# Performance work log

Hardware: AMD Instinct MI355X
Metric: run time of the kernel (lower is better)

Reference implementation:

```python
import jax, jax.numpy as jnp
import numpy as np

B, IN, H, OUT = 4096, 1024, 1024, 1024


def setup_inputs() -> dict:
    key = jax.random.key(0)
    ks = jax.random.split(key, 16)
    s_in = 1.0 / np.sqrt(IN)
    s_h = 1.0 / np.sqrt(H)
    d = {}
    d['input_vec'] = jax.random.normal(ks[0], (B, IN), jnp.float32)
    d['hidden_vec'] = jax.random.normal(ks[1], (B, H), jnp.float32)
    d['cell_vec'] = jax.random.normal(ks[2], (B, H), jnp.float32)
    names = ['f', 'i', 'o', 'g']
    for j, n in enumerate(names):
        d['Wx_' + n] = jax.random.uniform(ks[3 + 3 * j], (H, IN), jnp.float32, -s_in, s_in)
        d['bx_' + n] = jax.random.uniform(ks[4 + 3 * j], (H,), jnp.float32, -s_in, s_in)
        d['Wh_' + n] = jax.random.uniform(ks[5 + 3 * j], (H, H), jnp.float32, -s_h, s_h)
    d['W_out'] = jax.random.uniform(ks[15], (OUT, H), jnp.float32, -s_h, s_h)
    d['b_out'] = jax.random.uniform(jax.random.fold_in(key, 99), (OUT,), jnp.float32, -s_h, s_h)
    return d


def reference(input_vec, hidden_vec, cell_vec,
              Wx_f, bx_f, Wh_f,
              Wx_i, bx_i, Wh_i,
              Wx_o, bx_o, Wh_o,
              Wx_g, bx_g, Wh_g,
              W_out, b_out):
    # Fuse the 8 small linears into two GEMMs: [B,IN]x[IN,4H] and [B,H]x[H,4H].
    Wx = jnp.concatenate([Wx_f, Wx_i, Wx_o, Wx_g], axis=0)   # [4H, IN]
    Wh = jnp.concatenate([Wh_f, Wh_i, Wh_o, Wh_g], axis=0)   # [4H, H]
    b = jnp.concatenate([bx_f, bx_i, bx_o, bx_g], axis=0)    # [4H]
    gates = input_vec @ Wx.T + hidden_vec @ Wh.T + b          # [B, 4H]
    f, i, o, g = jnp.split(gates, 4, axis=1)
    f = jax.nn.sigmoid(f)
    i = jax.nn.sigmoid(i)
    o = jax.nn.sigmoid(o)
    g = jnp.tanh(g)
    new_cell = f * cell_vec + i * g
    new_hidden = o * jnp.tanh(new_cell)
    output_vec = new_hidden @ W_out.T + b_out
    return (new_hidden, new_cell, output_vec)
```

## Files before the change

### kernel.cpp

```cpp
#include <hip/hip_runtime.h>
#include <hip/hip_bf16.h>
#include <stdint.h>

#define B_   4096
#define IN_  1024
#define H_   1024
#define OUT_ 1024

typedef __attribute__((ext_vector_type(8)))  short short8;
typedef __attribute__((ext_vector_type(16))) float floatx16;

__device__ static inline void gload_lds16(const void* g, void* l) {
    __builtin_amdgcn_global_load_lds(
        (const __attribute__((address_space(1))) unsigned int*)g,
        (__attribute__((address_space(3))) unsigned int*)l,
        16, 0, 0);
}

__device__ static inline float sigmoidf_(float x) { return 1.0f / (1.0f + __expf(-x)); }
__device__ static inline float tanhf_(float x)    { return 1.0f - 2.0f / (1.0f + __expf(2.0f * x)); }

struct Ptrs8 { const float* p[8]; };

__global__ void cvt_all_kernel(const float* __restrict__ x, const float* __restrict__ h,
                               Ptrs8 ptrs, const float* __restrict__ wout,
                               __hip_bfloat16* __restrict__ xh,
                               __hip_bfloat16* __restrict__ Wc,
                               __hip_bfloat16* __restrict__ Wob) {
    int blk = blockIdx.x;
    const float* src;
    __hip_bfloat16* dst;
    if (blk < 8192) {
        int idx = blk * 256 + threadIdx.x;
        int b  = idx >> 9;
        int c4 = (idx & 511) * 4;
        src = (c4 < IN_) ? (x + (size_t)b * IN_ + c4)
                         : (h + (size_t)b * H_ + (c4 - IN_));
        dst = xh + (size_t)b * 2048 + c4;
    } else if (blk < 16384) {
        int idx = (blk - 8192) * 256 + threadIdx.x;
        int n  = idx >> 9;
        int c4 = (idx & 511) * 4;
        int gate = (n >> 5) & 3;
        int hh   = ((n >> 7) << 5) + (n & 31);
        src = (c4 < 1024) ? (ptrs.p[2 * gate]     + (size_t)hh * 1024 + c4)
                          : (ptrs.p[2 * gate + 1] + (size_t)hh * 1024 + (c4 - 1024));
        dst = Wc + (size_t)n * 2048 + c4;
    } else {
        int idx = (blk - 16384) * 256 + threadIdx.x;
        src = wout + (size_t)idx * 4;
        dst = Wob + (size_t)idx * 4;
    }
    float4 v = *(const float4*)src;
    dst[0] = __float2bfloat16(v.x);
    dst[1] = __float2bfloat16(v.y);
    dst[2] = __float2bfloat16(v.z);
    dst[3] = __float2bfloat16(v.w);
}

__global__ __launch_bounds__(512, 2) void gemm_gate_fused(
    const __hip_bfloat16* __restrict__ A,
    const __hip_bfloat16* __restrict__ Bm,
    const float* __restrict__ cell,
    const float* __restrict__ bxf, const float* __restrict__ bxi,
    const float* __restrict__ bxo, const float* __restrict__ bxg,
    float* __restrict__ new_hidden, float* __restrict__ new_cell,
    __hip_bfloat16* __restrict__ hb)
{
    constexpr int K = 2048;

    __shared__ short sA0[16384];
    __shared__ short sB0[16384];
    __shared__ short sA1[16384];
    __shared__ short sB1[16384];

    const int tid  = threadIdx.x;
    const int lane = tid & 63;
    const int wv   = tid >> 6;
    const int wr   = wv >> 1;
    const int wc   = wv & 1;

    const int bid    = blockIdx.x;
    const int xcd    = bid & 7;
    const int loc    = bid >> 3;
    const int n_tile = xcd * 2 + (loc & 1);
    const int m_tile = loc >> 1;
    const int m0 = m_tile * 256;
    const int n0 = n_tile * 256;

    const int srow   = tid >> 3;
    const int schunk = tid & 7;
    const int scg    = schunk ^ (srow & 7);
    const __hip_bfloat16* Ag = A  + (size_t)(m0 + srow) * K + scg * 8;
    const __hip_bfloat16* Bg = Bm + (size_t)(n0 + srow) * K + scg * 8;
    const int wvoff = wv * 1024;

    const int fr    = lane & 31;
    const int khalf = lane >> 5;
    const int sw    = fr & 7;

    int offA[2], offB[4];
    #pragma unroll
    for (int i = 0; i < 2; ++i) offA[i] = (wr * 64 + i * 32 + fr) * 128;
    #pragma unroll
    for (int j = 0; j < 4; ++j) offB[j] = (wc * 128 + j * 32 + fr) * 128;

    floatx16 acc[2][4] = {};

    #pragma unroll
    for (int s = 0; s < 4; ++s)
        gload_lds16(Ag + (size_t)(s * 64) * K, (char*)sA0 + s * 8192 + wvoff);
    #pragma unroll
    for (int s = 0; s < 4; ++s)
        gload_lds16(Bg + (size_t)(s * 64) * K, (char*)sB0 + s * 8192 + wvoff);
    asm volatile("s_waitcnt vmcnt(0)" ::: "memory");
    __builtin_amdgcn_s_barrier();
    __builtin_amdgcn_sched_barrier(0);

    auto tile_body = [&](const short* RA, const short* RB, short* WA, short* WB,
                         const __hip_bfloat16* Agt, const __hip_bfloat16* Bgt,
                         bool do_stage) {
        #pragma unroll
        for (int kk = 0; kk < 4; ++kk) {
            if (do_stage) {
                if (kk == 0) {
                    gload_lds16(Agt,                    (char*)WA + 0 * 8192 + wvoff);
                    gload_lds16(Agt + (size_t)64 * K,   (char*)WA + 1 * 8192 + wvoff);
                    gload_lds16(Bgt,                    (char*)WB + 0 * 8192 + wvoff);
                    gload_lds16(Bgt + (size_t)64 * K,   (char*)WB + 1 * 8192 + wvoff);
                } else if (kk == 1) {
                    gload_lds16(Agt + (size_t)128 * K,  (char*)WA + 2 * 8192 + wvoff);
                    gload_lds16(Agt + (size_t)192 * K,  (char*)WA + 3 * 8192 + wvoff);
                    gload_lds16(Bgt + (size_t)128 * K,  (char*)WB + 2 * 8192 + wvoff);
                    gload_lds16(Bgt + (size_t)192 * K,  (char*)WB + 3 * 8192 + wvoff);
                }
            }

            const int co = ((kk * 2 + khalf) ^ sw) * 16;
            short8 af[2], bfr[4];
            #pragma unroll
            for (int i = 0; i < 2; ++i)
                af[i] = *(const short8*)((const char*)RA + offA[i] + co);
            #pragma unroll
            for (int j = 0; j < 4; ++j)
                bfr[j] = *(const short8*)((const char*)RB + offB[j] + co);

            __builtin_amdgcn_s_barrier();
            __builtin_amdgcn_s_setprio(1);
            #pragma unroll
            for (int i = 0; i < 2; ++i)
                #pragma unroll
                for (int j = 0; j < 4; ++j)
                    acc[i][j] = __builtin_amdgcn_mfma_f32_32x32x16_bf16(af[i], bfr[j], acc[i][j], 0, 0, 0);
            __builtin_amdgcn_s_setprio(0);
            if (kk == 3)
                asm volatile("s_waitcnt vmcnt(0)" ::: "memory");
            __builtin_amdgcn_s_barrier();
            if (kk == 3)
                __builtin_amdgcn_sched_barrier(0);
        }
    };

    #pragma unroll 1
    for (int t2 = 0; t2 < 16; ++t2) {
        const int te = 2 * t2;
        tile_body(sA0, sB0, sA1, sB1,
                  Ag + (size_t)(te + 1) * 64, Bg + (size_t)(te + 1) * 64, true);
        tile_body(sA1, sB1, sA0, sB0,
                  Ag + (size_t)(te + 2) * 64, Bg + (size_t)(te + 2) * 64, t2 < 15);
    }

    const int h  = ((n0 + wc * 128) >> 2) + fr;
    const float bfb = bxf[h];
    const float bib = bxi[h];
    const float bob = bxo[h];
    const float bgb = bxg[h];

    #pragma unroll
    for (int i = 0; i < 2; ++i) {
        const int row_base = m0 + wr * 64 + i * 32 + 4 * khalf;
        #pragma unroll
        for (int reg = 0; reg < 16; ++reg) {
            const int row = row_base + (reg & 3) + 8 * (reg >> 2);
            const size_t off = (size_t)row * H_ + h;
            const float f  = sigmoidf_(acc[i][0][reg] + bfb);
            const float ii = sigmoidf_(acc[i][1][reg] + bib);
            const float o  = sigmoidf_(acc[i][2][reg] + bob);
            const float g  = tanhf_(acc[i][3][reg] + bgb);
            const float c  = f * cell[off] + ii * g;
            const float nh = o * tanhf_(c);
            new_cell[off]   = c;
            new_hidden[off] = nh;
            hb[off] = __float2bfloat16(nh);
        }
    }
}

__global__ __launch_bounds__(256, 2) void gemm_out(
    const __hip_bfloat16* __restrict__ A,
    const __hip_bfloat16* __restrict__ Bm,
    float* __restrict__ C,
    const float* __restrict__ bias)
{
    constexpr int BK = 64;
    constexpr int K  = 1024;
    constexpr int N  = 1024;

    __shared__ __hip_bfloat16 ldsA[128 * BK];
    __shared__ __hip_bfloat16 ldsB[64 * BK];

    const int tid  = threadIdx.x;
    const int lane = tid & 63;
    const int wv   = tid >> 6;

    const int bid    = blockIdx.x;
    const int xcd    = bid & 7;
    const int loc    = bid >> 3;
    const int n_tile = xcd * 2 + (loc & 1);
    const int m_tile = loc >> 1;
    const int m0 = m_tile * 128;
    const int n0 = n_tile * 64;

    const int srow   = tid >> 3;
    const int schunk = tid & 7;
    const int scg    = schunk ^ (srow & 7);
    const __hip_bfloat16* Ag = A  + (size_t)(m0 + srow) * K + scg * 8;
    const __hip_bfloat16* Bg = Bm + (size_t)(n0 + srow) * K + scg * 8;
    char* lA = (char*)ldsA + wv * 1024;
    char* lB = (char*)ldsB + wv * 1024;

    const int wrow  = wv * 32;
    const int fr    = lane & 31;
    const int khalf = lane >> 5;

    floatx16 acc[2] = {};

    for (int k0 = 0; k0 < K; k0 += BK) {
        #pragma unroll
        for (int s = 0; s < 4; ++s)
            gload_lds16(Ag + (size_t)(s * 32) * K + k0, lA + s * 4096);
        #pragma unroll
        for (int s = 0; s < 2; ++s)
            gload_lds16(Bg + (size_t)(s * 32) * K + k0, lB + s * 4096);
        __syncthreads();

        #pragma unroll
        for (int kk = 0; kk < 4; ++kk) {
            const int cg = kk * 2 + khalf;
            const int ra = wrow + fr;
            short8 af = *(const short8*)((const char*)ldsA + ra * 128 + ((cg ^ (ra & 7)) * 16));
            short8 bf[2];
            #pragma unroll
            for (int j = 0; j < 2; ++j) {
                const int r = j * 32 + fr;
                bf[j] = *(const short8*)((const char*)ldsB + r * 128 + ((cg ^ (r & 7)) * 16));
            }
            #pragma unroll
            for (int j = 0; j < 2; ++j)
                acc[j] = __builtin_amdgcn_mfma_f32_32x32x16_bf16(af, bf[j], acc[j], 0, 0, 0);
        }
        __syncthreads();
    }

    #pragma unroll
    for (int j = 0; j < 2; ++j) {
        const int col = n0 + j * 32 + fr;
        const float bb = bias[col];
        #pragma unroll
        for (int reg = 0; reg < 16; ++reg) {
            const int row = m0 + wrow + 4 * khalf + (reg & 3) + 8 * (reg >> 2);
            C[(size_t)row * N + col] = acc[j][reg] + bb;
        }
    }
}

extern "C" void kernel_launch(void* const* d_in, const int* in_sizes, int n_in,
                              void* d_out, int out_size, void* d_ws, size_t ws_size,
                              hipStream_t stream) {
    const float* input_vec  = (const float*)d_in[0];
    const float* hidden_vec = (const float*)d_in[1];
    const float* cell_vec   = (const float*)d_in[2];
    const float* Wx_f = (const float*)d_in[3];
    const float* bx_f = (const float*)d_in[4];
    const float* Wh_f = (const float*)d_in[5];
    const float* Wx_i = (const float*)d_in[6];
    const float* bx_i = (const float*)d_in[7];
    const float* Wh_i = (const float*)d_in[8];
    const float* Wx_o = (const float*)d_in[9];
    const float* bx_o = (const float*)d_in[10];
    const float* Wh_o = (const float*)d_in[11];
    const float* Wx_g = (const float*)d_in[12];
    const float* bx_g = (const float*)d_in[13];
    const float* Wh_g = (const float*)d_in[14];
    const float* W_out = (const float*)d_in[15];
    const float* b_out = (const float*)d_in[16];

    char* ws = (char*)d_ws;
    __hip_bfloat16* xh  = (__hip_bfloat16*)(ws);
    __hip_bfloat16* Wc  = (__hip_bfloat16*)(ws + (16ull << 20));
    __hip_bfloat16* Wob = (__hip_bfloat16*)(ws + (32ull << 20));
    __hip_bfloat16* hb  = (__hip_bfloat16*)(ws + (34ull << 20));

    float* new_hidden = (float*)d_out;
    float* new_cell   = new_hidden + (size_t)B_ * H_;
    float* out_vec    = new_cell + (size_t)B_ * H_;

    Ptrs8 p;
    p.p[0] = Wx_f; p.p[1] = Wh_f; p.p[2] = Wx_i; p.p[3] = Wh_i;
    p.p[4] = Wx_o; p.p[5] = Wh_o; p.p[6] = Wx_g; p.p[7] = Wh_g;
    cvt_all_kernel<<<17408, 256, 0, stream>>>(input_vec, hidden_vec, p, W_out, xh, Wc, Wob);

    gemm_gate_fused<<<256, 512, 0, stream>>>(
        xh, Wc, cell_vec, bx_f, bx_i, bx_o, bx_g, new_hidden, new_cell, hb);

    gemm_out<<<512, 256, 0, stream>>>(hb, Wob, out_vec, b_out);
}
```

Measured before the change: 249.8 us.

## Use 4 waves with 128x128 per-wave tiles and one barrier per K-tile

The gate GEMM now launches 256 threads instead of 512, and each wave accumulates a 128x128 output block with a 4x4 grid of MFMA accumulators instead of 2x4. All global-to-LDS staging for the next K-tile is issued at the start of each tile body, and the per-kk barriers and priority switches are replaced by a single wait-and-barrier at the end of each tile. The aim is more register-level reuse of LDS fragments and less synchronisation overhead. The cost is much higher register pressure, fewer waves available to hide latency, and the launch bounds drop to one block per CU.

```diff
diff --git a/kernel.cpp b/kernel.cpp
--- a/kernel.cpp
+++ b/kernel.cpp
@@ -58,7 +58,7 @@
     dst[3] = __float2bfloat16(v.w);
 }
 
-__global__ __launch_bounds__(512, 2) void gemm_gate_fused(
+__global__ __launch_bounds__(256, 1) void gemm_gate_fused(
     const __hip_bfloat16* __restrict__ A,
     const __hip_bfloat16* __restrict__ Bm,
     const float* __restrict__ cell,
@@ -99,76 +99,63 @@
     const int khalf = lane >> 5;
     const int sw    = fr & 7;
 
-    int offA[2], offB[4];
-    #pragma unroll
-    for (int i = 0; i < 2; ++i) offA[i] = (wr * 64 + i * 32 + fr) * 128;
+    int offA[4], offB[4];
+    #pragma unroll
+    for (int i = 0; i < 4; ++i) offA[i] = (wr * 128 + i * 32 + fr) * 128;
     #pragma unroll
     for (int j = 0; j < 4; ++j) offB[j] = (wc * 128 + j * 32 + fr) * 128;
 
-    floatx16 acc[2][4] = {};
-
-    #pragma unroll
-    for (int s = 0; s < 4; ++s)
-        gload_lds16(Ag + (size_t)(s * 64) * K, (char*)sA0 + s * 8192 + wvoff);
-    #pragma unroll
-    for (int s = 0; s < 4; ++s)
-        gload_lds16(Bg + (size_t)(s * 64) * K, (char*)sB0 + s * 8192 + wvoff);
+    floatx16 acc[4][4] = {};
+
+    #pragma unroll
+    for (int s = 0; s < 8; ++s) {
+        gload_lds16(Ag + (size_t)(s * 32) * K, (char*)sA0 + s * 4096 + wvoff);
+        gload_lds16(Bg + (size_t)(s * 32) * K, (char*)sB0 + s * 4096 + wvoff);
+    }
     asm volatile("s_waitcnt vmcnt(0)" ::: "memory");
     __builtin_amdgcn_s_barrier();
     __builtin_amdgcn_sched_barrier(0);
 
-    auto tile_body = [&](const short* RA, const short* RB, short* WA, short* WB,
-                         const __hip_bfloat16* Agt, const __hip_bfloat16* Bgt,
-                         bool do_stage) {
-        #pragma unroll
-        for (int kk = 0; kk < 4; ++kk) {
-            if (do_stage) {
-                if (kk == 0) {
-                    gload_lds16(Agt,                    (char*)WA + 0 * 8192 + wvoff);
-                    gload_lds16(Agt + (size_t)64 * K,   (char*)WA + 1 * 8192 + wvoff);
-                    gload_lds16(Bgt,                    (char*)WB + 0 * 8192 + wvoff);
-                    gload_lds16(Bgt + (size_t)64 * K,   (char*)WB + 1 * 8192 + wvoff);
-                } else if (kk == 1) {
-                    gload_lds16(Agt + (size_t)128 * K,  (char*)WA + 2 * 8192 + wvoff);
-                    gload_lds16(Agt + (size_t)192 * K,  (char*)WA + 3 * 8192 + wvoff);
-                    gload_lds16(Bgt + (size_t)128 * K,  (char*)WB + 2 * 8192 + wvoff);
-                    gload_lds16(Bgt + (size_t)192 * K,  (char*)WB + 3 * 8192 + wvoff);
-                }
-            }
-
-            const int co = ((kk * 2 + khalf) ^ sw) * 16;
-            short8 af[2], bfr[4];
-            #pragma unroll
-            for (int i = 0; i < 2; ++i)
-                af[i] = *(const short8*)((const char*)RA + offA[i] + co);
-            #pragma unroll
-            for (int j = 0; j < 4; ++j)
-                bfr[j] = *(const short8*)((const char*)RB + offB[j] + co);
-
-            __builtin_amdgcn_s_barrier();
-            __builtin_amdgcn_s_setprio(1);
-            #pragma unroll
-            for (int i = 0; i < 2; ++i)
-                #pragma unroll
-                for (int j = 0; j < 4; ++j)
-                    acc[i][j] = __builtin_amdgcn_mfma_f32_32x32x16_bf16(af[i], bfr[j], acc[i][j], 0, 0, 0);
-            __builtin_amdgcn_s_setprio(0);
-            if (kk == 3)
-                asm volatile("s_waitcnt vmcnt(0)" ::: "memory");
-            __builtin_amdgcn_s_barrier();
-            if (kk == 3)
-                __builtin_amdgcn_sched_barrier(0);
-        }
-    };
+#define TILE_BODY(RA, RB, WA, WB, tnext, DO_STAGE)                                        \
+    {                                                                                     \
+        if (DO_STAGE) {                                                                   \
+            const __hip_bfloat16* Agt = Ag + (size_t)(tnext) * 64;                        \
+            const __hip_bfloat16* Bgt = Bg + (size_t)(tnext) * 64;                        \
+            _Pragma("unroll")                                                             \
+            for (int s = 0; s < 8; ++s) {                                                 \
+                gload_lds16(Agt + (size_t)(s * 32) * K, (char*)(WA) + s * 4096 + wvoff);  \
+                gload_lds16(Bgt + (size_t)(s * 32) * K, (char*)(WB) + s * 4096 + wvoff);  \
+            }                                                                             \
+            __builtin_amdgcn_sched_barrier(0);                                            \
+        }                                                                                 \
+        _Pragma("unroll")                                                                 \
+        for (int kk = 0; kk < 4; ++kk) {                                                  \
+            const int co = ((kk * 2 + khalf) ^ sw) * 16;                                  \
+            short8 af[4], bfr[4];                                                         \
+            _Pragma("unroll")                                                             \
+            for (int i = 0; i < 4; ++i)                                                   \
+                af[i]  = *(const short8*)((const char*)(RA) + offA[i] + co);              \
+            _Pragma("unroll")                                                             \
+            for (int j = 0; j < 4; ++j)                                                   \
+                bfr[j] = *(const short8*)((const char*)(RB) + offB[j] + co);              \
+            _Pragma("unroll")                                                             \
+            for (int i = 0; i < 4; ++i)                                                   \
+                _Pragma("unroll")                                                         \
+                for (int j = 0; j < 4; ++j)                                               \
+                    acc[i][j] = __builtin_amdgcn_mfma_f32_32x32x16_bf16(                  \
+                        af[i], bfr[j], acc[i][j], 0, 0, 0);                               \
+        }                                                                                 \
+        asm volatile("s_waitcnt vmcnt(0)" ::: "memory");                                  \
+        __builtin_amdgcn_s_barrier();                                                     \
+        __builtin_amdgcn_sched_barrier(0);                                                \
+    }
 
     #pragma unroll 1
     for (int t2 = 0; t2 < 16; ++t2) {
-        const int te = 2 * t2;
-        tile_body(sA0, sB0, sA1, sB1,
-                  Ag + (size_t)(te + 1) * 64, Bg + (size_t)(te + 1) * 64, true);
-        tile_body(sA1, sB1, sA0, sB0,
-                  Ag + (size_t)(te + 2) * 64, Bg + (size_t)(te + 2) * 64, t2 < 15);
-    }
+        TILE_BODY(sA0, sB0, sA1, sB1, 2 * t2 + 1, true);
+        TILE_BODY(sA1, sB1, sA0, sB0, 2 * t2 + 2, (t2 < 15));
+    }
+#undef TILE_BODY
 
     const int h  = ((n0 + wc * 128) >> 2) + fr;
     const float bfb = bxf[h];
@@ -177,8 +164,8 @@
     const float bgb = bxg[h];
 
     #pragma unroll
-    for (int i = 0; i < 2; ++i) {
-        const int row_base = m0 + wr * 64 + i * 32 + 4 * khalf;
+    for (int i = 0; i < 4; ++i) {
+        const int row_base = m0 + wr * 128 + i * 32 + 4 * khalf;
         #pragma unroll
         for (int reg = 0; reg < 16; ++reg) {
             const int row = row_base + (reg & 3) + 8 * (reg >> 2);
@@ -310,7 +297,7 @@
     p.p[4] = Wx_o; p.p[5] = Wh_o; p.p[6] = Wx_g; p.p[7] = Wh_g;
     cvt_all_kernel<<<17408, 256, 0, stream>>>(input_vec, hidden_vec, p, W_out, xh, Wc, Wob);
 
-    gemm_gate_fused<<<256, 512, 0, stream>>>(
+    gemm_gate_fused<<<256, 256, 0, stream>>>(
         xh, Wc, cell_vec, bx_f, bx_i, bx_o, bx_g, new_hidden, new_cell, hb);
 
     gemm_out<<<512, 256, 0, stream>>>(hb, Wob, out_vec, b_out);
```

After: 289.2 us. 1.16x slower.
